# Optimization experiments

Measured on AMD Instinct MI355X. Metric: run time of the kernel, lower is better.

## Reference

```python
import jax, jax.numpy as jnp
import numpy as np

N_QUBITS = 4
N_LAYERS = 2
DIM = 1 << N_QUBITS  # 16-dim state vector

# --- fixed (parameter-free) CNOT entangler layers, precomputed as 16x16 permutations ---

def _cnot_perm(c, t):
    M = np.zeros((DIM, DIM), np.complex64)
    for b in range(DIM):
        b2 = b ^ (1 << (N_QUBITS - 1 - t)) if (b >> (N_QUBITS - 1 - c)) & 1 else b
        M[b2, b] = 1.0
    return M

def _entangler(r):
    E = np.eye(DIM, dtype=np.complex64)
    for i in range(N_QUBITS):  # pennylane applies CNOT(i, (i+r)%n) sequentially
        E = _cnot_perm(i, (i + r) % N_QUBITS) @ E
    return E

ENT = [jnp.asarray(_entangler((l % (N_QUBITS - 1)) + 1)) for l in range(N_LAYERS)]
# Z_TABLE[b, w] = <b| Z_w |b>
Z_TABLE = jnp.asarray(np.array([[1.0 - 2.0 * ((b >> (N_QUBITS - 1 - w)) & 1) for w in range(N_QUBITS)] for b in range(DIM)], np.float32))


def _rot(phi, theta, omega):
    # pennylane Rot = RZ(omega) @ RY(theta) @ RZ(phi)
    c = jnp.cos(theta / 2).astype(jnp.complex64)
    s = jnp.sin(theta / 2).astype(jnp.complex64)
    a = jnp.exp(-0.5j * (phi + omega)) * c
    b = -jnp.exp(0.5j * (phi - omega)) * s
    cc = jnp.exp(-0.5j * (phi - omega)) * s
    d = jnp.exp(0.5j * (phi + omega)) * c
    return jnp.stack([jnp.stack([a, b]), jnp.stack([cc, d])])


def _vqc_unitary(weights):
    # weights: [N_LAYERS, N_QUBITS, 3] -> 16x16 unitary for StronglyEntanglingLayers
    U = jnp.eye(DIM, dtype=jnp.complex64)
    for l in range(N_LAYERS):
        R = _rot(weights[l, 0, 0], weights[l, 0, 1], weights[l, 0, 2])
        for q in range(1, N_QUBITS):  # wire 0 is most-significant bit -> left kron factor
            R = jnp.kron(R, _rot(weights[l, q, 0], weights[l, q, 1], weights[l, q, 2]))
        U = ENT[l] @ (R @ U)
    return U


def _vqc(x, weights):
    # x: [..., 4] rotation angles; AngleEmbedding uses RX: RX(a)|0> = [cos(a/2), -i sin(a/2)]
    c = jnp.cos(x / 2).astype(jnp.complex64)
    s = jnp.sin(x / 2).astype(jnp.complex64)
    amp = jnp.stack([c, -1j * s], axis=-1)  # [..., 4, 2]
    psi0 = jnp.einsum('...a,...b,...c,...d->...abcd', amp[..., 0, :], amp[..., 1, :], amp[..., 2, :], amp[..., 3, :])
    psi0 = psi0.reshape(x.shape[:-1] + (DIM,))
    U = _vqc_unitary(weights)
    psi = jnp.einsum('ij,...j->...i', U, psi0)
    probs = psi.real ** 2 + psi.imag ** 2
    return probs @ Z_TABLE  # [..., 4] PauliZ expectation values


def setup_inputs() -> dict:
    key = jax.random.key(0)
    k0, k1, k2, k3 = jax.random.split(key, 4)
    H = 768
    B, S = 8, 2048
    embeddings = jax.random.normal(k0, (B, S, H), dtype=jnp.float32)
    lim = 1.0 / np.sqrt(H)
    Wq = jax.random.normal(k1, (N_QUBITS, H), dtype=jnp.float32) * lim
    Wk = jax.random.normal(k2, (N_QUBITS, H), dtype=jnp.float32) * lim
    bq = jnp.zeros((N_QUBITS,), jnp.float32)
    bk = jnp.zeros((N_QUBITS,), jnp.float32)
    vqc_weights = jax.random.uniform(k3, (N_LAYERS, N_QUBITS, 3), dtype=jnp.float32) * (2.0 * np.pi)
    return {'embeddings': embeddings, 'Wq': Wq, 'bq': bq, 'Wk': Wk, 'bk': bk, 'vqc_weights': vqc_weights}


def reference(embeddings, Wq, bq, Wk, bk, vqc_weights):
    Q = jnp.einsum('bsh,qh->bsq', embeddings, Wq) + bq  # [B,S,4]
    K = jnp.einsum('bsh,qh->bsq', embeddings, Wk) + bk
    Qv = _vqc(Q, vqc_weights)  # [B,S,4]
    Kv = _vqc(K, vqc_weights)
    attn = jax.nn.softmax(jnp.einsum('bsq,btq->bst', Qv, Kv), axis=-1)  # [B,S,S]
    return jnp.einsum('bst,bth->bsh', attn, embeddings)
```

## Files before the change

kernel.cpp:

```cpp
#include <hip/hip_runtime.h>

#define NB 8
#define NS 2048
#define NH 768
#define NPOS (NB*NS)

typedef _Float16 half8 __attribute__((ext_vector_type(8)));
typedef float floatx4 __attribute__((ext_vector_type(4)));

#define GLOAD_LDS16(gp, lp) __builtin_amdgcn_global_load_lds( \
  (const __attribute__((address_space(1))) unsigned int*)(gp), \
  (__attribute__((address_space(3))) unsigned int*)(lp), 16, 0, 0)

__global__ __launch_bounds__(384) void epre_kernel(
    const float* __restrict__ E, const float* __restrict__ wts,
    float* __restrict__ Vre, float* __restrict__ Vim,
    unsigned short* __restrict__ ET) {
  int tc = blockIdx.x, hb = blockIdx.y, b = blockIdx.z;
  int tid = threadIdx.x;

  if (tc == 0 && hb == 0 && b == 0 && tid < 16) {
    int j = tid;
    float ar[16], ai[16];
#pragma unroll
    for (int i = 0; i < 16; i++) { ar[i] = (i == j) ? 1.f : 0.f; ai[i] = 0.f; }
#pragma unroll
    for (int l = 0; l < 2; l++) {
#pragma unroll
      for (int q = 0; q < 4; q++) {
        float phi = wts[(l*4+q)*3+0];
        float th  = wts[(l*4+q)*3+1];
        float om  = wts[(l*4+q)*3+2];
        float ct = cosf(0.5f*th), st = sinf(0.5f*th);
        float sm = 0.5f*(phi+om), df = 0.5f*(phi-om);
        float cs = cosf(sm), ss = sinf(sm), cd = cosf(df), sd = sinf(df);
        float Ar =  cs*ct, Ai = -ss*ct;
        float Br = -cd*st, Bi = -sd*st;
        float Cr =  cd*st, Ci = -sd*st;
        float Dr =  cs*ct, Di =  ss*ct;
        int pb = 1 << (3-q);
#pragma unroll
        for (int b0 = 0; b0 < 16; b0++) {
          if (b0 & pb) continue;
          int b1 = b0 | pb;
          float xr = ar[b0], xi = ai[b0], yr = ar[b1], yi = ai[b1];
          ar[b0] = Ar*xr - Ai*xi + Br*yr - Bi*yi;
          ai[b0] = Ar*xi + Ai*xr + Br*yi + Bi*yr;
          ar[b1] = Cr*xr - Ci*xi + Dr*yr - Di*yi;
          ai[b1] = Cr*xi + Ci*xr + Dr*yi + Di*yr;
        }
      }
      const int r = (l == 0) ? 1 : 2;
#pragma unroll
      for (int i2 = 0; i2 < 4; i2++) {
        int cb = 1 << (3-i2);
        int tb = 1 << (3-((i2+r)&3));
#pragma unroll
        for (int b0 = 0; b0 < 16; b0++) {
          if ((b0 & cb) && !(b0 & tb)) {
            int b1 = b0 | tb;
            float tr = ar[b0], ti = ai[b0];
            ar[b0] = ar[b1]; ai[b0] = ai[b1];
            ar[b1] = tr;     ai[b1] = ti;
          }
        }
      }
    }
    int pc = __popc((unsigned)j) & 3;
#pragma unroll
    for (int i = 0; i < 16; i++) {
      float vr = ar[i], vi = ai[i], orr, oi;
      if      (pc == 0) { orr =  vr; oi =  vi; }
      else if (pc == 1) { orr =  vi; oi = -vr; }
      else if (pc == 2) { orr = -vr; oi = -vi; }
      else              { orr = -vi; oi =  vr; }
      Vre[i*16+j] = orr;
      Vim[i*16+j] = oi;
    }
  }

  size_t tbase = ((size_t)((b*4 + hb)*64 + tc)) * 12288;
  const float* Eb = E + (size_t)b*NS*NH + (size_t)tc*32*NH + hb*192;
#pragma unroll
  for (int u = 0; u < 2; u++) {
    int unit = tid + 384*u;
    int q2 = unit / 192, h2 = unit % 192;
    unsigned hi4[4], lo4[4];
#pragma unroll
    for (int jp = 0; jp < 4; jp++) {
      float ea = Eb[(size_t)(q2*8 + 2*jp    )*NH + h2];
      float eb = Eb[(size_t)(q2*8 + 2*jp + 1)*NH + h2];
      _Float16 ha = (_Float16)ea, hb16 = (_Float16)eb;
      float la = ea - (float)ha, lb = eb - (float)hb16;
      unsigned uha = __builtin_bit_cast(unsigned short, ha);
      unsigned uhb = __builtin_bit_cast(unsigned short, hb16);
      unsigned ula = __builtin_bit_cast(unsigned short, (_Float16)la);
      unsigned ulb = __builtin_bit_cast(unsigned short, (_Float16)lb);
      hi4[jp] = uha | (uhb << 16);
      lo4[jp] = ula | (ulb << 16);
    }
    int off = h2*32 + ((q2 ^ ((h2>>1)&3))*8);
    *(uint4*)&ET[tbase + off]        = make_uint4(hi4[0],hi4[1],hi4[2],hi4[3]);
    *(uint4*)&ET[tbase + 6144 + off] = make_uint4(lo4[0],lo4[1],lo4[2],lo4[3]);
  }
}

__global__ __launch_bounds__(256) void proj_vqc_kernel(
    const float* __restrict__ E, const float* __restrict__ Wq, const float* __restrict__ bq,
    const float* __restrict__ Wk, const float* __restrict__ bk,
    const float* __restrict__ Vre, const float* __restrict__ Vim,
    float* __restrict__ Qv, float* __restrict__ Kv) {
  __shared__ __align__(16) float WqL[768*4];
  __shared__ __align__(16) float WkL[768*4];
  __shared__ float Vsh[2][16*17];
  int tid = threadIdx.x;
  for (int idx = tid; idx < 768*4; idx += 256) {
    int e = idx >> 2, w = idx & 3;
    WqL[e*4+w] = Wq[w*768+e];
    WkL[e*4+w] = Wk[w*768+e];
  }
  if (tid < 256) {
    int i = tid >> 4, jj = tid & 15;
    Vsh[0][i*17+jj] = Vre[tid];
    Vsh[1][i*17+jj] = Vim[tid];
  }
  __syncthreads();
  float bqr0=bq[0], bqr1=bq[1], bqr2=bq[2], bqr3=bq[3];
  float bkr0=bk[0], bkr1=bk[1], bkr2=bk[2], bkr3=bk[3];
  int lane = tid & 63;
  int wid  = blockIdx.x*4 + (tid >> 6);
  int nw   = gridDim.x*4;
  int grp  = lane >> 4;
  int i    = lane & 15;
  for (int pos = wid; pos < NPOS; pos += nw) {
    const float* er = E + (size_t)pos*768;
    float pq[4] = {0.f,0.f,0.f,0.f};
    float pk[4] = {0.f,0.f,0.f,0.f};
#pragma unroll
    for (int k2 = 0; k2 < 3; k2++) {
      float4 ev = *(const float4*)(er + lane*4 + 256*k2);
#pragma unroll
      for (int jj = 0; jj < 4; jj++) {
        int e = lane*4 + 256*k2 + jj;
        float evs = (jj==0) ? ev.x : (jj==1) ? ev.y : (jj==2) ? ev.z : ev.w;
        float4 wq4 = *(const float4*)&WqL[e*4];
        float4 wk4 = *(const float4*)&WkL[e*4];
        pq[0] += evs*wq4.x; pq[1] += evs*wq4.y; pq[2] += evs*wq4.z; pq[3] += evs*wq4.w;
        pk[0] += evs*wk4.x; pk[1] += evs*wk4.y; pk[2] += evs*wk4.z; pk[3] += evs*wk4.w;
      }
    }
    float part[8];
#pragma unroll
    for (int w = 0; w < 8; w++) {
      float v = (w < 4) ? pq[w] : pk[w-4];
      v += __shfl_xor(v, 32); v += __shfl_xor(v, 16); v += __shfl_xor(v, 8);
      v += __shfl_xor(v, 4);  v += __shfl_xor(v, 2);  v += __shfl_xor(v, 1);
      part[w] = v;
    }
    if (grp < 2) {
      float a0,a1,a2,a3;
      if (grp == 0) { a0=part[0]+bqr0; a1=part[1]+bqr1; a2=part[2]+bqr2; a3=part[3]+bqr3; }
      else          { a0=part[4]+bkr0; a1=part[5]+bkr1; a2=part[6]+bkr2; a3=part[7]+bkr3; }
      float c0=cosf(0.5f*a0), s0=sinf(0.5f*a0);
      float c1=cosf(0.5f*a1), s1=sinf(0.5f*a1);
      float c2=cosf(0.5f*a2), s2=sinf(0.5f*a2);
      float c3=cosf(0.5f*a3), s3=sinf(0.5f*a3);
      float m[16];
#pragma unroll
      for (int j2 = 0; j2 < 16; j2++) {
        float f0 = (j2 & 8) ? s0 : c0;
        float f1 = (j2 & 4) ? s1 : c1;
        float f2 = (j2 & 2) ? s2 : c2;
        float f3 = (j2 & 1) ? s3 : c3;
        m[j2] = f0*f1*f2*f3;
      }
      float re = 0.f, im = 0.f;
#pragma unroll
      for (int j2 = 0; j2 < 16; j2++) {
        re += Vsh[0][i*17+j2]*m[j2];
        im += Vsh[1][i*17+j2]*m[j2];
      }
      float pr = re*re + im*im;
      float r0 = (i & 8) ? -pr : pr;
      float r1 = (i & 4) ? -pr : pr;
      float r2 = (i & 2) ? -pr : pr;
      float r3 = (i & 1) ? -pr : pr;
#pragma unroll
      for (int off = 8; off >= 1; off >>= 1) {
        r0 += __shfl_xor(r0, off);
        r1 += __shfl_xor(r1, off);
        r2 += __shfl_xor(r2, off);
        r3 += __shfl_xor(r3, off);
      }
      if (i == 0) {
        float* dst = (grp == 0 ? Qv : Kv) + (size_t)pos*4;
        dst[0]=r0; dst[1]=r1; dst[2]=r2; dst[3]=r3;
      }
    }
  }
}

#define TKC 32

__global__ __launch_bounds__(512, 4) void attn_kernel(
    const unsigned short* __restrict__ ET, const float* __restrict__ Qv,
    const float* __restrict__ Kv, float* __restrict__ out) {
  int sblk = blockIdx.x;
  int hblk = blockIdx.y;
  int b    = blockIdx.z;
  int tid  = threadIdx.x;
  int lane = tid & 63;
  int w    = tid >> 6;

  __shared__ __align__(16) unsigned short sA[2][4096];
  __shared__ __align__(16) unsigned short sB[2][12288];
  __shared__ float denp[128*4];
  __shared__ float dfin[128];

  const unsigned short* tE = ET + ((size_t)((b*4 + hblk)*64)) * 12288;
  const float* Kvb = Kv + (size_t)b*NS*4;

  int sP = tid & 127, qP = tid >> 7;
  float4 qv = *(const float4*)&Qv[((size_t)(b*NS + sblk*128) + sP)*4];
  float den_acc = 0.f;
  int offA = sP*32 + ((qP ^ ((sP>>1)&3))*8);

  int sh = w & 1, hh = w >> 1;
  floatx4 acc[4][3];
#pragma unroll
  for (int i = 0; i < 4; i++)
#pragma unroll
    for (int jt = 0; jt < 3; jt++) acc[i][jt] = floatx4{0.f,0.f,0.f,0.f};

  int m16 = lane & 15, q16 = lane >> 4;
  int cidx = (q16 ^ ((m16 >> 1) & 3)) * 8;
  int t16 = tid * 8;

  auto kvload = [&](int tb, float4* kvr) {
    const float* kvp = Kvb + (size_t)(tb + qP*8)*4;
#pragma unroll
    for (int j = 0; j < 8; j++) kvr[j] = *(const float4*)(kvp + j*4);
  };

  auto pcompute = [&](const float4* kvr) -> uint4 {
    unsigned h4[4];
    float dsum = 0.f;
#pragma unroll
    for (int jp = 0; jp < 4; jp++) {
      float4 ka = kvr[2*jp];
      float4 kb = kvr[2*jp+1];
      float arga = qv.x*ka.x + qv.y*ka.y + qv.z*ka.z + qv.w*ka.w;
      float argb = qv.x*kb.x + qv.y*kb.y + qv.z*kb.z + qv.w*kb.w;
      float pa = __expf(arga), pb = __expf(argb);
      dsum += pa + pb;
      unsigned ua = (unsigned)__builtin_bit_cast(unsigned short, (_Float16)pa);
      unsigned ub = (unsigned)__builtin_bit_cast(unsigned short, (_Float16)pb);
      h4[jp] = ua | (ub << 16);
    }
    den_acc += dsum;
    return make_uint4(h4[0], h4[1], h4[2], h4[3]);
  };

  auto do_mfma = [&](const unsigned short* sAc, const unsigned short* sBc) {
    half8 a[4];
#pragma unroll
    for (int i = 0; i < 4; i++) {
      int srow = sh*64 + i*16 + m16;
      a[i] = __builtin_bit_cast(half8, *(const uint4*)&sAc[srow*TKC + cidx]);
    }
#pragma unroll
    for (int jt = 0; jt < 3; jt++) {
      int hrow = hh*48 + jt*16 + m16;
      half8 bh_ = __builtin_bit_cast(half8, *(const uint4*)&sBc[hrow*TKC + cidx]);
      half8 bl_ = __builtin_bit_cast(half8, *(const uint4*)&sBc[6144 + hrow*TKC + cidx]);
#pragma unroll
      for (int i = 0; i < 4; i++) {
        acc[i][jt] = __builtin_amdgcn_mfma_f32_16x16x32_f16(a[i], bl_, acc[i][jt], 0, 0, 0);
        acc[i][jt] = __builtin_amdgcn_mfma_f32_16x16x32_f16(a[i], bh_, acc[i][jt], 0, 0, 0);
      }
    }
  };

  {
    float4 kvr[8];
    kvload(0, kvr);
    GLOAD_LDS16(tE + t16,        &sB[0][0] + t16);
    GLOAD_LDS16(tE + 4096 + t16, &sB[0][0] + 4096 + t16);
    GLOAD_LDS16(tE + 8192 + t16, &sB[0][0] + 8192 + t16);
    uint4 ph = pcompute(kvr);
    *(uint4*)&sA[0][offA] = ph;
  }

  for (int ci = 0; ci < 64; ci++) {
    int cb = ci & 1;
    __syncthreads();
    if (ci < 63) {
      float4 kvr[8];
      kvload((ci+1)*TKC, kvr);
      const unsigned short* nE = tE + (size_t)(ci+1)*12288;
      unsigned short* sBn = &sB[cb^1][0];
      GLOAD_LDS16(nE + t16,        sBn + t16);
      GLOAD_LDS16(nE + 4096 + t16, sBn + 4096 + t16);
      GLOAD_LDS16(nE + 8192 + t16, sBn + 8192 + t16);
      uint4 ph = pcompute(kvr);
      *(uint4*)&sA[cb^1][offA] = ph;
    }
    do_mfma(&sA[cb][0], &sB[cb][0]);
  }

  __syncthreads();
  denp[sP*4 + qP] = den_acc;
  __syncthreads();
  if (tid < 128) {
    dfin[tid] = denp[tid*4] + denp[tid*4+1] + denp[tid*4+2] + denp[tid*4+3];
  }
  __syncthreads();

  float* ob = out + ((size_t)(b*NS + sblk*128))*NH + hblk*192;
#pragma unroll
  for (int i = 0; i < 4; i++) {
#pragma unroll
    for (int reg = 0; reg < 4; reg++) {
      int row = q16*4 + reg;
      int s_loc = sh*64 + i*16 + row;
      float invd = 1.0f / dfin[s_loc];
#pragma unroll
      for (int jt = 0; jt < 3; jt++) {
        int h_loc = hh*48 + jt*16 + m16;
        ob[(size_t)s_loc*NH + h_loc] = acc[i][jt][reg] * invd;
      }
    }
  }
}

extern "C" void kernel_launch(void* const* d_in, const int* in_sizes, int n_in,
                              void* d_out, int out_size, void* d_ws, size_t ws_size,
                              hipStream_t stream) {
  const float* E   = (const float*)d_in[0];
  const float* Wq  = (const float*)d_in[1];
  const float* bq  = (const float*)d_in[2];
  const float* Wk  = (const float*)d_in[3];
  const float* bk  = (const float*)d_in[4];
  const float* wts = (const float*)d_in[5];
  float* ws  = (float*)d_ws;
  float* Vre = ws;
  float* Vim = ws + 256;
  float* Qv  = ws + 512;
  float* Kv  = Qv + (size_t)NPOS*4;
  unsigned short* ET = (unsigned short*)(Kv + (size_t)NPOS*4);
  float* out = (float*)d_out;

  epre_kernel<<<dim3(64, 4, 8), 384, 0, stream>>>(E, wts, Vre, Vim, ET);
  proj_vqc_kernel<<<1024, 256, 0, stream>>>(E, Wq, bq, Wk, bk, Vre, Vim, Qv, Kv);
  attn_kernel<<<dim3(16, 4, 8), 512, 0, stream>>>(ET, Qv, Kv, out);
}
```

Measured before the change: 258.8 us.

## Precompute softmax numerators in separate kernel and stream them into attention

Adds a pgen kernel that computes exp(Qv·Kv) as fp16 tiles plus partial denominators once per (batch, s-block). The attention kernel then loads those tiles into LDS with async global-to-LDS copies instead of recomputing them in each of the four h-blocks, and it drops the in-kernel denominator reduction. The grid is also flattened with batch as the fastest index, which changes block scheduling and cache locality. The cost is an extra kernel launch and a 64 MB fp16 P buffer that has to be written and then read back.

```diff
diff --git a/kernel.cpp b/kernel.cpp
--- a/kernel.cpp
+++ b/kernel.cpp
@@ -200,30 +200,62 @@
   }
 }
 
+__global__ __launch_bounds__(512) void pgen_kernel(
+    const float* __restrict__ Qv, const float* __restrict__ Kv,
+    unsigned short* __restrict__ P, float* __restrict__ Den) {
+  int th = blockIdx.x, sblk = blockIdx.y, b = blockIdx.z;
+  int tid = threadIdx.x;
+  int s = tid >> 2, qq = tid & 3;
+  int q = qq ^ ((s >> 1) & 3);
+  float4 qv = *(const float4*)&Qv[((size_t)(b*NS + sblk*128) + s)*4];
+  const float* Kvb = Kv + (size_t)b*NS*4;
+  unsigned short* Pt = P + ((size_t)(b*16 + sblk))*64*4096;
+  float den_acc = 0.f;
+  for (int tc = th*32; tc < th*32 + 32; tc++) {
+    const float* kvp = Kvb + ((size_t)tc*32 + q*8)*4;
+    unsigned h4[4];
+#pragma unroll
+    for (int jp = 0; jp < 4; jp++) {
+      float4 ka = *(const float4*)(kvp + 8*jp);
+      float4 kb = *(const float4*)(kvp + 8*jp + 4);
+      float arga = qv.x*ka.x + qv.y*ka.y + qv.z*ka.z + qv.w*ka.w;
+      float argb = qv.x*kb.x + qv.y*kb.y + qv.z*kb.z + qv.w*kb.w;
+      float pa = __expf(arga), pb = __expf(argb);
+      den_acc += pa + pb;
+      unsigned ua = (unsigned)__builtin_bit_cast(unsigned short, (_Float16)pa);
+      unsigned ub = (unsigned)__builtin_bit_cast(unsigned short, (_Float16)pb);
+      h4[jp] = ua | (ub << 16);
+    }
+    *(uint4*)&Pt[(size_t)tc*4096 + tid*8] = make_uint4(h4[0], h4[1], h4[2], h4[3]);
+  }
+  float v = den_acc;
+  v += __shfl_xor(v, 1);
+  v += __shfl_xor(v, 2);
+  if (qq == 0) {
+    Den[(size_t)th*NPOS + (size_t)b*NS + sblk*128 + s] = v;
+  }
+}
+
 #define TKC 32
 
 __global__ __launch_bounds__(512, 4) void attn_kernel(
-    const unsigned short* __restrict__ ET, const float* __restrict__ Qv,
-    const float* __restrict__ Kv, float* __restrict__ out) {
-  int sblk = blockIdx.x;
-  int hblk = blockIdx.y;
-  int b    = blockIdx.z;
+    const unsigned short* __restrict__ ET, const unsigned short* __restrict__ P,
+    const float* __restrict__ Den, float* __restrict__ out) {
+  int bid  = blockIdx.x;
+  int b    = bid & 7;
+  int r    = bid >> 3;
+  int sblk = r & 15;
+  int hblk = r >> 4;
   int tid  = threadIdx.x;
   int lane = tid & 63;
   int w    = tid >> 6;
 
-  __shared__ __align__(16) unsigned short sA[2][4096];
+  __shared__ __align__(16) unsigned short sPt[2][4096];
   __shared__ __align__(16) unsigned short sB[2][12288];
-  __shared__ float denp[128*4];
   __shared__ float dfin[128];
 
   const unsigned short* tE = ET + ((size_t)((b*4 + hblk)*64)) * 12288;
-  const float* Kvb = Kv + (size_t)b*NS*4;
-
-  int sP = tid & 127, qP = tid >> 7;
-  float4 qv = *(const float4*)&Qv[((size_t)(b*NS + sblk*128) + sP)*4];
-  float den_acc = 0.f;
-  int offA = sP*32 + ((qP ^ ((sP>>1)&3))*8);
+  const unsigned short* tP = P + ((size_t)(b*16 + sblk))*64*4096;
 
   int sh = w & 1, hh = w >> 1;
   floatx4 acc[4][3];
@@ -236,32 +268,29 @@
   int cidx = (q16 ^ ((m16 >> 1) & 3)) * 8;
   int t16 = tid * 8;
 
-  auto kvload = [&](int tb, float4* kvr) {
-    const float* kvp = Kvb + (size_t)(tb + qP*8)*4;
-#pragma unroll
-    for (int j = 0; j < 8; j++) kvr[j] = *(const float4*)(kvp + j*4);
-  };
-
-  auto pcompute = [&](const float4* kvr) -> uint4 {
-    unsigned h4[4];
-    float dsum = 0.f;
-#pragma unroll
-    for (int jp = 0; jp < 4; jp++) {
-      float4 ka = kvr[2*jp];
-      float4 kb = kvr[2*jp+1];
-      float arga = qv.x*ka.x + qv.y*ka.y + qv.z*ka.z + qv.w*ka.w;
-      float argb = qv.x*kb.x + qv.y*kb.y + qv.z*kb.z + qv.w*kb.w;
-      float pa = __expf(arga), pb = __expf(argb);
-      dsum += pa + pb;
-      unsigned ua = (unsigned)__builtin_bit_cast(unsigned short, (_Float16)pa);
-      unsigned ub = (unsigned)__builtin_bit_cast(unsigned short, (_Float16)pb);
-      h4[jp] = ua | (ub << 16);
-    }
-    den_acc += dsum;
-    return make_uint4(h4[0], h4[1], h4[2], h4[3]);
-  };
-
-  auto do_mfma = [&](const unsigned short* sAc, const unsigned short* sBc) {
+  if (tid < 128) {
+    size_t di = (size_t)b*NS + sblk*128 + tid;
+    dfin[tid] = Den[di] + Den[(size_t)NPOS + di];
+  }
+  GLOAD_LDS16(tE + t16,        &sB[0][0] + t16);
+  GLOAD_LDS16(tE + 4096 + t16, &sB[0][0] + 4096 + t16);
+  GLOAD_LDS16(tE + 8192 + t16, &sB[0][0] + 8192 + t16);
+  GLOAD_LDS16(tP + t16,        &sPt[0][0] + t16);
+
+  for (int ci = 0; ci < 64; ci++) {
+    int cb = ci & 1;
+    __syncthreads();
+    if (ci < 63) {
+      const unsigned short* nE = tE + (size_t)(ci+1)*12288;
+      const unsigned short* nP = tP + (size_t)(ci+1)*4096;
+      unsigned short* sBn = &sB[cb^1][0];
+      GLOAD_LDS16(nE + t16,        sBn + t16);
+      GLOAD_LDS16(nE + 4096 + t16, sBn + 4096 + t16);
+      GLOAD_LDS16(nE + 8192 + t16, sBn + 8192 + t16);
+      GLOAD_LDS16(nP + t16,        &sPt[cb^1][0] + t16);
+    }
+    const unsigned short* sAc = &sPt[cb][0];
+    const unsigned short* sBc = &sB[cb][0];
     half8 a[4];
 #pragma unroll
     for (int i = 0; i < 4; i++) {
@@ -279,42 +308,7 @@
         acc[i][jt] = __builtin_amdgcn_mfma_f32_16x16x32_f16(a[i], bh_, acc[i][jt], 0, 0, 0);
       }
     }
-  };
-
-  {
-    float4 kvr[8];
-    kvload(0, kvr);
-    GLOAD_LDS16(tE + t16,        &sB[0][0] + t16);
-    GLOAD_LDS16(tE + 4096 + t16, &sB[0][0] + 4096 + t16);
-    GLOAD_LDS16(tE + 8192 + t16, &sB[0][0] + 8192 + t16);
-    uint4 ph = pcompute(kvr);
-    *(uint4*)&sA[0][offA] = ph;
-  }
-
-  for (int ci = 0; ci < 64; ci++) {
-    int cb = ci & 1;
-    __syncthreads();
-    if (ci < 63) {
-      float4 kvr[8];
-      kvload((ci+1)*TKC, kvr);
-      const unsigned short* nE = tE + (size_t)(ci+1)*12288;
-      unsigned short* sBn = &sB[cb^1][0];
-      GLOAD_LDS16(nE + t16,        sBn + t16);
-      GLOAD_LDS16(nE + 4096 + t16, sBn + 4096 + t16);
-      GLOAD_LDS16(nE + 8192 + t16, sBn + 8192 + t16);
-      uint4 ph = pcompute(kvr);
-      *(uint4*)&sA[cb^1][offA] = ph;
-    }
-    do_mfma(&sA[cb][0], &sB[cb][0]);
-  }
-
-  __syncthreads();
-  denp[sP*4 + qP] = den_acc;
-  __syncthreads();
-  if (tid < 128) {
-    dfin[tid] = denp[tid*4] + denp[tid*4+1] + denp[tid*4+2] + denp[tid*4+3];
-  }
-  __syncthreads();
+  }
 
   float* ob = out + ((size_t)(b*NS + sblk*128))*NH + hblk*192;
 #pragma unroll
@@ -347,10 +341,13 @@
   float* Vim = ws + 256;
   float* Qv  = ws + 512;
   float* Kv  = Qv + (size_t)NPOS*4;
-  unsigned short* ET = (unsigned short*)(Kv + (size_t)NPOS*4);
+  float* Den = Kv + (size_t)NPOS*4;
+  unsigned short* ET = (unsigned short*)(Den + (size_t)2*NPOS);
+  unsigned short* P  = ET + (size_t)NB*4*64*12288;
   float* out = (float*)d_out;
 
   epre_kernel<<<dim3(64, 4, 8), 384, 0, stream>>>(E, wts, Vre, Vim, ET);
   proj_vqc_kernel<<<1024, 256, 0, stream>>>(E, Wq, bq, Wk, bk, Vre, Vim, Qv, Kv);
-  attn_kernel<<<dim3(16, 4, 8), 512, 0, stream>>>(ET, Qv, Kv, out);
-}
+  pgen_kernel<<<dim3(2, 16, 8), 512, 0, stream>>>(Qv, Kv, P, Den);
+  attn_kernel<<<dim3(512), 512, 0, stream>>>(ET, P, Den, out);
+}
```

New measurement: 275.2 us. 6.3% more time.

## Double attention H-tile per block to halve exp recomputation and grid size

Applied to the files above, without the earlier changes.

Each attention block now covers 384 hidden columns instead of 192, with six accumulator tiles per wave. This halves the redundant exp/probability computation, which was previously repeated for each of four H-blocks. It also changes the thread-to-A-slot mapping so the denominator reduces through two shuffles instead of an LDS round trip, and flattens the grid so blocks of the same batch sit adjacent. The grid drops to 256 blocks with higher register use and double the LDS staging, so occupancy drops to two blocks per CU and the machine is less filled.

```diff
diff --git a/kernel.cpp b/kernel.cpp
--- a/kernel.cpp
+++ b/kernel.cpp
@@ -202,42 +202,45 @@
 
 #define TKC 32
 
-__global__ __launch_bounds__(512, 4) void attn_kernel(
+__global__ __launch_bounds__(512, 2) void attn_kernel(
     const unsigned short* __restrict__ ET, const float* __restrict__ Qv,
     const float* __restrict__ Kv, float* __restrict__ out) {
-  int sblk = blockIdx.x;
-  int hblk = blockIdx.y;
-  int b    = blockIdx.z;
+  int bid  = blockIdx.x;
+  int b    = bid & 7;
+  int r    = bid >> 3;
+  int sblk = r & 15;
+  int hp   = r >> 4;
   int tid  = threadIdx.x;
   int lane = tid & 63;
   int w    = tid >> 6;
 
   __shared__ __align__(16) unsigned short sA[2][4096];
-  __shared__ __align__(16) unsigned short sB[2][12288];
-  __shared__ float denp[128*4];
+  __shared__ __align__(16) unsigned short sB[2][24576];
   __shared__ float dfin[128];
 
-  const unsigned short* tE = ET + ((size_t)((b*4 + hblk)*64)) * 12288;
-  const float* Kvb = Kv + (size_t)b*NS*4;
-
-  int sP = tid & 127, qP = tid >> 7;
-  float4 qv = *(const float4*)&Qv[((size_t)(b*NS + sblk*128) + sP)*4];
+  const unsigned short* tEh = ET + ((size_t)((b*4 + hp*2)*64)) * 12288;
+
+  int sPg = tid >> 2, slotg = tid & 3;
+  int qg  = slotg ^ ((sPg >> 1) & 3);
+  int offA = sPg*32 + slotg*8;
+  float4 qv = *(const float4*)&Qv[((size_t)(b*NS + sblk*128) + sPg)*4];
+  const float* kvbase = Kv + (size_t)b*NS*4 + (size_t)qg*8*4;
   float den_acc = 0.f;
-  int offA = sP*32 + ((qP ^ ((sP>>1)&3))*8);
 
   int sh = w & 1, hh = w >> 1;
-  floatx4 acc[4][3];
+  floatx4 acc[4][6];
 #pragma unroll
   for (int i = 0; i < 4; i++)
 #pragma unroll
-    for (int jt = 0; jt < 3; jt++) acc[i][jt] = floatx4{0.f,0.f,0.f,0.f};
+    for (int jt = 0; jt < 6; jt++) acc[i][jt] = floatx4{0.f,0.f,0.f,0.f};
 
   int m16 = lane & 15, q16 = lane >> 4;
   int cidx = (q16 ^ ((m16 >> 1) & 3)) * 8;
   int t16 = tid * 8;
-
-  auto kvload = [&](int tb, float4* kvr) {
-    const float* kvp = Kvb + (size_t)(tb + qP*8)*4;
+  int hbase = (hh >> 1)*12288 + (hh & 1)*3072;
+
+  auto kvload = [&](int ci, float4* kvr) {
+    const float* kvp = kvbase + (size_t)ci*128;
 #pragma unroll
     for (int j = 0; j < 8; j++) kvr[j] = *(const float4*)(kvp + j*4);
   };
@@ -261,32 +264,22 @@
     return make_uint4(h4[0], h4[1], h4[2], h4[3]);
   };
 
-  auto do_mfma = [&](const unsigned short* sAc, const unsigned short* sBc) {
-    half8 a[4];
-#pragma unroll
-    for (int i = 0; i < 4; i++) {
-      int srow = sh*64 + i*16 + m16;
-      a[i] = __builtin_bit_cast(half8, *(const uint4*)&sAc[srow*TKC + cidx]);
-    }
-#pragma unroll
-    for (int jt = 0; jt < 3; jt++) {
-      int hrow = hh*48 + jt*16 + m16;
-      half8 bh_ = __builtin_bit_cast(half8, *(const uint4*)&sBc[hrow*TKC + cidx]);
-      half8 bl_ = __builtin_bit_cast(half8, *(const uint4*)&sBc[6144 + hrow*TKC + cidx]);
-#pragma unroll
-      for (int i = 0; i < 4; i++) {
-        acc[i][jt] = __builtin_amdgcn_mfma_f32_16x16x32_f16(a[i], bl_, acc[i][jt], 0, 0, 0);
-        acc[i][jt] = __builtin_amdgcn_mfma_f32_16x16x32_f16(a[i], bh_, acc[i][jt], 0, 0, 0);
-      }
-    }
+  auto dma_chunk = [&](int ci, int nb) {
+    const unsigned short* t0 = tEh + (size_t)ci*12288;
+    const unsigned short* t1 = t0 + (size_t)64*12288;
+    unsigned short* d = &sB[nb][0];
+    GLOAD_LDS16(t0 + t16,        d + t16);
+    GLOAD_LDS16(t0 + 4096 + t16, d + 4096 + t16);
+    GLOAD_LDS16(t0 + 8192 + t16, d + 8192 + t16);
+    GLOAD_LDS16(t1 + t16,        d + 12288 + t16);
+    GLOAD_LDS16(t1 + 4096 + t16, d + 16384 + t16);
+    GLOAD_LDS16(t1 + 8192 + t16, d + 20480 + t16);
   };
 
   {
     float4 kvr[8];
     kvload(0, kvr);
-    GLOAD_LDS16(tE + t16,        &sB[0][0] + t16);
-    GLOAD_LDS16(tE + 4096 + t16, &sB[0][0] + 4096 + t16);
-    GLOAD_LDS16(tE + 8192 + t16, &sB[0][0] + 8192 + t16);
+    dma_chunk(0, 0);
     uint4 ph = pcompute(kvr);
     *(uint4*)&sA[0][offA] = ph;
   }
@@ -296,27 +289,41 @@
     __syncthreads();
     if (ci < 63) {
       float4 kvr[8];
-      kvload((ci+1)*TKC, kvr);
-      const unsigned short* nE = tE + (size_t)(ci+1)*12288;
-      unsigned short* sBn = &sB[cb^1][0];
-      GLOAD_LDS16(nE + t16,        sBn + t16);
-      GLOAD_LDS16(nE + 4096 + t16, sBn + 4096 + t16);
-      GLOAD_LDS16(nE + 8192 + t16, sBn + 8192 + t16);
+      kvload(ci+1, kvr);
+      dma_chunk(ci+1, cb^1);
       uint4 ph = pcompute(kvr);
       *(uint4*)&sA[cb^1][offA] = ph;
     }
-    do_mfma(&sA[cb][0], &sB[cb][0]);
-  }
-
+    const unsigned short* sAc = &sA[cb][0];
+    const unsigned short* sBc = &sB[cb][0];
+    half8 a[4];
+#pragma unroll
+    for (int i = 0; i < 4; i++) {
+      int srow = sh*64 + i*16 + m16;
+      a[i] = __builtin_bit_cast(half8, *(const uint4*)&sAc[srow*TKC + cidx]);
+    }
+#pragma unroll
+    for (int jt = 0; jt < 6; jt++) {
+      int ro = hbase + (jt*16 + m16)*TKC + cidx;
+      half8 bh_ = __builtin_bit_cast(half8, *(const uint4*)&sBc[ro]);
+      half8 bl_ = __builtin_bit_cast(half8, *(const uint4*)&sBc[ro + 6144]);
+#pragma unroll
+      for (int i = 0; i < 4; i++) {
+        acc[i][jt] = __builtin_amdgcn_mfma_f32_16x16x32_f16(a[i], bl_, acc[i][jt], 0, 0, 0);
+        acc[i][jt] = __builtin_amdgcn_mfma_f32_16x16x32_f16(a[i], bh_, acc[i][jt], 0, 0, 0);
+      }
+    }
+  }
+
+  {
+    float v = den_acc;
+    v += __shfl_xor(v, 1);
+    v += __shfl_xor(v, 2);
+    if (slotg == 0) dfin[sPg] = v;
+  }
   __syncthreads();
-  denp[sP*4 + qP] = den_acc;
-  __syncthreads();
-  if (tid < 128) {
-    dfin[tid] = denp[tid*4] + denp[tid*4+1] + denp[tid*4+2] + denp[tid*4+3];
-  }
-  __syncthreads();
-
-  float* ob = out + ((size_t)(b*NS + sblk*128))*NH + hblk*192;
+
+  float* ob = out + ((size_t)(b*NS + sblk*128))*NH + hp*384;
 #pragma unroll
   for (int i = 0; i < 4; i++) {
 #pragma unroll
@@ -325,8 +332,8 @@
       int s_loc = sh*64 + i*16 + row;
       float invd = 1.0f / dfin[s_loc];
 #pragma unroll
-      for (int jt = 0; jt < 3; jt++) {
-        int h_loc = hh*48 + jt*16 + m16;
+      for (int jt = 0; jt < 6; jt++) {
+        int h_loc = hh*96 + jt*16 + m16;
         ob[(size_t)s_loc*NH + h_loc] = acc[i][jt][reg] * invd;
       }
     }
@@ -352,5 +359,5 @@
 
   epre_kernel<<<dim3(64, 4, 8), 384, 0, stream>>>(E, wts, Vre, Vim, ET);
   proj_vqc_kernel<<<1024, 256, 0, stream>>>(E, Wq, bq, Wk, bk, Vre, Vim, Qv, Kv);
-  attn_kernel<<<dim3(16, 4, 8), 512, 0, stream>>>(ET, Qv, Kv, out);
+  attn_kernel<<<dim3(256), 512, 0, stream>>>(ET, Qv, Kv, out);
 }
```

Measured after the change: 338.6 us. 1.31x slower.
